# Performance work log

Hardware: AMD Instinct MI355X
Metric: run time of the kernel (lower is better)

## Reference

```python
import jax, jax.numpy as jnp
import numpy as np

N_NODES = 100000
N_EDGES = 1600000
IN_DIM = 128
HEADS = 8
STATE_DIM = 16   # per-head hidden
OUT_DIM = 8      # per-head output
NEG_SLOPE = 0.2


def _gat_conv(x, src, dst, W, a_src, a_dst, b, num_nodes, heads, d):
    # x: [N, F_in]; W: [F_in, heads*d]; a_src/a_dst: [heads, d]; b: [heads*d]
    h = (x @ W).reshape(num_nodes, heads, d)                # [N,H,D]
    s_src = jnp.einsum('nhd,hd->nh', h, a_src)              # [N,H]
    s_dst = jnp.einsum('nhd,hd->nh', h, a_dst)              # [N,H]
    e = jax.nn.leaky_relu(s_src[src] + s_dst[dst], NEG_SLOPE)   # [E,H]
    # segment softmax over edges sharing the same destination node
    m = jax.ops.segment_max(e, dst, num_segments=num_nodes)     # [N,H]
    m = jnp.where(jnp.isfinite(m), m, jnp.zeros_like(m))
    ex = jnp.exp(e - m[dst])                                    # [E,H]
    denom = jax.ops.segment_sum(ex, dst, num_segments=num_nodes)
    alpha = ex / (denom[dst] + 1e-16)                           # [E,H]
    # weighted scatter-aggregate of source features
    out = jax.ops.segment_sum(h[src] * alpha[:, :, None], dst, num_segments=num_nodes)
    return out.reshape(num_nodes, heads * d) + b


def setup_inputs() -> dict:
    key = jax.random.key(0)
    ks = jax.random.split(key, 12)
    x = jax.random.normal(ks[0], (N_NODES, IN_DIM), dtype=jnp.float32)
    edge_index = jax.random.randint(ks[1], (2, N_EDGES), 0, N_NODES, dtype=jnp.int64)
    s1 = 1.0 / np.sqrt(IN_DIM)
    s2 = 1.0 / np.sqrt(HEADS * STATE_DIM)
    W1 = jax.random.normal(ks[2], (IN_DIM, HEADS * STATE_DIM), dtype=jnp.float32) * s1
    a1_src = jax.random.normal(ks[3], (HEADS, STATE_DIM), dtype=jnp.float32) * s2
    a1_dst = jax.random.normal(ks[4], (HEADS, STATE_DIM), dtype=jnp.float32) * s2
    b1 = jnp.zeros((HEADS * STATE_DIM,), dtype=jnp.float32)
    W2 = jax.random.normal(ks[5], (HEADS * STATE_DIM, HEADS * OUT_DIM), dtype=jnp.float32) * s2
    a2_src = jax.random.normal(ks[6], (HEADS, OUT_DIM), dtype=jnp.float32) * s2
    a2_dst = jax.random.normal(ks[7], (HEADS, OUT_DIM), dtype=jnp.float32) * s2
    b2 = jnp.zeros((HEADS * OUT_DIM,), dtype=jnp.float32)
    return {"x": x, "edge_index": edge_index, "W1": W1, "a1_src": a1_src,
            "a1_dst": a1_dst, "b1": b1, "W2": W2, "a2_src": a2_src,
            "a2_dst": a2_dst, "b2": b2}


def reference(x, edge_index, W1, a1_src, a1_dst, b1, W2, a2_src, a2_dst, b2):
    # PyG GATConv adds self-loops by default
    loops = jnp.arange(N_NODES, dtype=edge_index.dtype)
    src = jnp.concatenate([edge_index[0], loops])
    dst = jnp.concatenate([edge_index[1], loops])
    h = _gat_conv(x, src, dst, W1, a1_src, a1_dst, b1, N_NODES, HEADS, STATE_DIM)
    h = jax.nn.relu(h)  # dropout is identity at eval
    out = _gat_conv(h, src, dst, W2, a2_src, a2_dst, b2, N_NODES, HEADS, OUT_DIM)
    return out  # [N, HEADS*OUT_DIM]
```

## Files before the change

kernel.cpp:

```cpp
#include <hip/hip_runtime.h>
#include <hip/hip_fp16.h>
#include <math.h>

#define N_NODES 100000
#define N_EDGES 1600000
#define IN_DIM 128
#define HEADS 8
#define D1 16
#define D2 8
#define NEG_SLOPE 0.2f

#define NBKT ((N_NODES + 255) / 256)
#define PART_CHUNK 4096
#define BCAP 6144
#define BCSTRIDE 32
#define GEMM1_BLOCKS ((N_NODES + 63) / 64)

typedef _Float16 f16x8 __attribute__((ext_vector_type(8)));
typedef float    f32x4 __attribute__((ext_vector_type(4)));

struct __align__(16) half8 { __half2 a, b, c, d; };

__device__ __forceinline__ f16x8 load_cvt8(const float* p) {
    float4 v0 = *(const float4*)p, v1 = *(const float4*)(p + 4);
    f16x8 r;
    r[0] = (_Float16)v0.x; r[1] = (_Float16)v0.y;
    r[2] = (_Float16)v0.z; r[3] = (_Float16)v0.w;
    r[4] = (_Float16)v1.x; r[5] = (_Float16)v1.y;
    r[6] = (_Float16)v1.z; r[7] = (_Float16)v1.w;
    return r;
}

template<int CTRL>
__device__ __forceinline__ float dpp_add(float x) {
    int y = __builtin_amdgcn_update_dpp(0, __builtin_bit_cast(int, x),
                                        CTRL, 0xF, 0xF, true);
    return x + __builtin_bit_cast(float, y);
}

template<int OUTC, int D, bool XF32>
__device__ __forceinline__ void gemm_body(int gb, const void* __restrict__ Ain,
                                          const __half* __restrict__ Bt,
                                          __half* __restrict__ C,
                                          const float* __restrict__ a_s,
                                          const float* __restrict__ a_d,
                                          float* __restrict__ s_src,
                                          float* __restrict__ s_dst,
                                          int n_rows) {
    constexpr int K = 128;
    constexpr int NT = OUTC / 16;
    int wid  = threadIdx.x >> 6;
    int lane = threadIdx.x & 63;
    int row0 = gb * 64 + wid * 16;
    int lr   = lane & 15;
    int ks   = (lane >> 4) * 8;

    int arow = row0 + lr;
    arow = arow < n_rows ? arow : n_rows - 1;

    f16x8 a0, a1, a2, a3;
    if constexpr (XF32) {
        const float* ap = (const float*)Ain + (long)arow * K + ks;
        a0 = load_cvt8(ap);
        a1 = load_cvt8(ap + 32);
        a2 = load_cvt8(ap + 64);
        a3 = load_cvt8(ap + 96);
    } else {
        const __half* ap = (const __half*)Ain + (long)arow * K + ks;
        a0 = *(const f16x8*)(ap);
        a1 = *(const f16x8*)(ap + 32);
        a2 = *(const f16x8*)(ap + 64);
        a3 = *(const f16x8*)(ap + 96);
    }

    f32x4 acc[NT];
#pragma unroll
    for (int j = 0; j < NT; ++j) acc[j] = (f32x4)(0.f);

#pragma unroll
    for (int j = 0; j < NT; ++j) {
        const __half* bp = Bt + (long)(j * 16 + lr) * K + ks;
        f16x8 b0 = *(const f16x8*)(bp);
        f16x8 b1 = *(const f16x8*)(bp + 32);
        f16x8 b2 = *(const f16x8*)(bp + 64);
        f16x8 b3 = *(const f16x8*)(bp + 96);
        acc[j] = __builtin_amdgcn_mfma_f32_16x16x32_f16(a0, b0, acc[j], 0, 0, 0);
        acc[j] = __builtin_amdgcn_mfma_f32_16x16x32_f16(a1, b1, acc[j], 0, 0, 0);
        acc[j] = __builtin_amdgcn_mfma_f32_16x16x32_f16(a2, b2, acc[j], 0, 0, 0);
        acc[j] = __builtin_amdgcn_mfma_f32_16x16x32_f16(a3, b3, acc[j], 0, 0, 0);
    }

    float asv[NT], adv[NT];
#pragma unroll
    for (int j = 0; j < NT; ++j) {
        asv[j] = a_s[j * 16 + lr];
        adv[j] = a_d[j * 16 + lr];
    }

    __shared__ __half stg[4][16 * OUTC];
    __half* sp_ = stg[wid];

    int rbase4 = (lane >> 4) * 4;
#pragma unroll
    for (int r = 0; r < 4; ++r) {
        int lrow = rbase4 + r;

#pragma unroll
        for (int j = 0; j < NT; ++j)
            sp_[lrow * OUTC + j * 16 + lr] = __float2half(acc[j][r]);

        int rr = row0 + lrow;
        bool valid = rr < n_rows;

        float ps[NT], pd[NT];
#pragma unroll
        for (int j = 0; j < NT; ++j) {
            ps[j] = acc[j][r] * asv[j];
            pd[j] = acc[j][r] * adv[j];
        }
        if constexpr (D == 16) {
#pragma unroll
            for (int j = 0; j < NT; ++j) {
                ps[j] = dpp_add<0x118>(ps[j]); ps[j] = dpp_add<0x114>(ps[j]);
                ps[j] = dpp_add<0x112>(ps[j]); ps[j] = dpp_add<0x111>(ps[j]);
                pd[j] = dpp_add<0x118>(pd[j]); pd[j] = dpp_add<0x114>(pd[j]);
                pd[j] = dpp_add<0x112>(pd[j]); pd[j] = dpp_add<0x111>(pd[j]);
            }
            if (valid && lr == 15) {
                float* sp = s_src + rr * 8;
                float* dp = s_dst + rr * 8;
                *(float4*)(sp)     = make_float4(ps[0], ps[1], ps[2], ps[3]);
                *(float4*)(sp + 4) = make_float4(ps[4], ps[5], ps[6], ps[7]);
                *(float4*)(dp)     = make_float4(pd[0], pd[1], pd[2], pd[3]);
                *(float4*)(dp + 4) = make_float4(pd[4], pd[5], pd[6], pd[7]);
            }
        } else {
#pragma unroll
            for (int j = 0; j < NT; ++j) {
                ps[j] = dpp_add<0x114>(ps[j]); ps[j] = dpp_add<0x112>(ps[j]);
                ps[j] = dpp_add<0x111>(ps[j]);
                pd[j] = dpp_add<0x114>(pd[j]); pd[j] = dpp_add<0x112>(pd[j]);
                pd[j] = dpp_add<0x111>(pd[j]);
            }
            if (valid && lr == 7) {
#pragma unroll
                for (int j = 0; j < NT; ++j) {
                    s_src[rr * 8 + 2 * j] = ps[j];
                    s_dst[rr * 8 + 2 * j] = pd[j];
                }
            }
            if (valid && lr == 15) {
#pragma unroll
                for (int j = 0; j < NT; ++j) {
                    s_src[rr * 8 + 2 * j + 1] = ps[j];
                    s_dst[rr * 8 + 2 * j + 1] = pd[j];
                }
            }
        }
    }

    constexpr int CPR = OUTC / 8;
    constexpr int CPL = 2 * OUTC / 64;
#pragma unroll
    for (int t = 0; t < CPL; ++t) {
        int c = t * 64 + lane;
        int row = c / CPR;
        if (row0 + row < n_rows) {
            half8 v = *(half8*)(sp_ + c * 8);
            *(half8*)(C + (long)row0 * OUTC + c * 8) = v;
        }
    }
}

__global__ __launch_bounds__(256)
void convert_w_kernel(const float* __restrict__ W1, const float* __restrict__ W2,
                      __half* __restrict__ Wt1, __half* __restrict__ Wt2,
                      int* __restrict__ bcursor) {
    int idx = blockIdx.x * 256 + threadIdx.x;
    if (idx < NBKT * BCSTRIDE) bcursor[idx] = 0;
    if (idx < 128 * 128) {
        int k = idx / 128, j = idx % 128;
        Wt1[(long)j * 128 + k] = __float2half(W1[idx]);
    } else {
        int i = idx - 128 * 128;
        if (i < 128 * 64) {
            int k = i / 64, j = i % 64;
            Wt2[(long)j * 128 + k] = __float2half(W2[i]);
        }
    }
}

__global__ __launch_bounds__(256)
void partition_kernel(const int* __restrict__ src, const int* __restrict__ dst,
                      int* __restrict__ bcursor, int2* __restrict__ bpairs) {
    constexpr int EPT = PART_CHUNK / 256;
    __shared__ int hist[NBKT];
    for (int i = threadIdx.x; i < NBKT; i += 256) hist[i] = 0;
    __syncthreads();
    int e0 = blockIdx.x * PART_CHUNK;
    int sv[EPT], dv[EPT];
#pragma unroll
    for (int j = 0; j < EPT; ++j) {
        int e = e0 + j * 256 + threadIdx.x;
        bool ok = e < N_EDGES;
        dv[j] = ok ? dst[e] : -1;
        sv[j] = ok ? src[e] : 0;
    }
#pragma unroll
    for (int j = 0; j < EPT; ++j)
        if (dv[j] >= 0) atomicAdd(&hist[dv[j] >> 8], 1);
    __syncthreads();
    for (int i = threadIdx.x; i < NBKT; i += 256) {
        int c = hist[i];
        if (c) {
            int r = atomicAdd(&bcursor[i * BCSTRIDE], c);
            hist[i] = i * BCAP + (r < BCAP ? r : BCAP);
        }
    }
    __syncthreads();
#pragma unroll
    for (int j = 0; j < EPT; ++j) {
        if (dv[j] >= 0) {
            int bkt = dv[j] >> 8;
            int pos = atomicAdd(&hist[bkt], 1);
            if (pos < (bkt + 1) * BCAP)
                bpairs[pos] = make_int2(sv[j], dv[j]);
        }
    }
}

__global__ __launch_bounds__(256)
void localcsr_gemm1_kernel(const int* __restrict__ bcursor,
                           const int2* __restrict__ bpairs,
                           int* __restrict__ row_start, int* __restrict__ row_end,
                           int* __restrict__ eidx,
                           const float* __restrict__ x, const __half* __restrict__ Wt1,
                           __half* __restrict__ C,
                           const float* __restrict__ a_s, const float* __restrict__ a_d,
                           float* __restrict__ s_src, float* __restrict__ s_dst) {
    if (blockIdx.x >= NBKT) {
        gemm_body<128, D1, true>(blockIdx.x - NBKT, x, Wt1, C,
                                 a_s, a_d, s_src, s_dst, N_NODES);
        return;
    }
    __shared__ int cnt[256];
    __shared__ int sh[256];
    __shared__ int cur[256];
    int b = blockIdx.x;
    int tid = threadIdx.x;
    int n0 = b << 8;
    int m0 = b * BCAP;
    int count = bcursor[b * BCSTRIDE];
    int m1 = m0 + (count < BCAP ? count : BCAP);
    cnt[tid] = 0;
    __syncthreads();
    for (int k = m0 + tid; k < m1; k += 256)
        atomicAdd(&cnt[bpairs[k].y & 255], 1);
    __syncthreads();
    int c = cnt[tid];
    sh[tid] = c;
    __syncthreads();
    int run = c;
    for (int off = 1; off < 256; off <<= 1) {
        int add = (tid >= off) ? sh[tid - off] : 0;
        __syncthreads();
        run += add;
        sh[tid] = run;
        __syncthreads();
    }
    int excl = run - c;
    cur[tid] = m0 + excl;
    if (n0 + tid < N_NODES) {
        row_start[n0 + tid] = m0 + excl;
        row_end[n0 + tid]   = m0 + excl + c;
    }
    __syncthreads();
    for (int k = m0 + tid; k < m1; k += 256) {
        int2 p = bpairs[k];
        int pos = atomicAdd(&cur[p.y & 255], 1);
        eidx[pos] = p.x;
    }
}

__global__ __launch_bounds__(256)
void gemm2_kernel(const __half* __restrict__ A, const __half* __restrict__ Bt,
                  __half* __restrict__ C,
                  const float* __restrict__ a_s, const float* __restrict__ a_d,
                  float* __restrict__ s_src, float* __restrict__ s_dst) {
    gemm_body<64, D2, false>(blockIdx.x, A, Bt, C, a_s, a_d, s_src, s_dst, N_NODES);
}

template<int D, bool RELU, typename OT>
__global__ __launch_bounds__(256)
void aggregate_wave_kernel(const int* __restrict__ rs, const int* __restrict__ re,
                           const int* __restrict__ eidx,
                           const __half* __restrict__ h,
                           const float* __restrict__ ssrc, const float* __restrict__ sdst,
                           const float* __restrict__ bias, OT* __restrict__ out) {
    constexpr int F = HEADS * D;
    constexpr int EPL = F / 64;
    int lane = threadIdx.x & 63;
    int node = blockIdx.x * (256 / 64) + (threadIdx.x >> 6);
    node = __builtin_amdgcn_readfirstlane(node);
    if (node >= N_NODES) return;
    int hd = lane >> 3;
    int esl = lane & 7;

    float sdv = sdst[node * HEADS + hd];
    float sc0 = ssrc[node * HEADS + hd] + sdv;
    float w0 = __expf(sc0 > 0.f ? sc0 : NEG_SLOPE * sc0);
    float wsum = w0;

    float accx, accy = 0.f;
    if constexpr (EPL == 2) {
        float2 v = __half22float2(*(const __half2*)(h + (long)node * F + lane * 2));
        accx = w0 * v.x; accy = w0 * v.y;
    } else {
        accx = w0 * __half2float(h[(long)node * F + lane]);
    }

    int e0 = rs[node], e1 = re[node];
    int e1m1 = e1 - 1;

    for (int e = e0; e < e1; e += 8) {
        int idx = e + esl;
        int ci = idx < e1m1 ? idx : e1m1;
        int s_mine = eidx[ci];
        float sc = ssrc[s_mine * HEADS + hd] + sdv;
        float w_mine = __expf(sc > 0.f ? sc : NEG_SLOPE * sc);
        w_mine = (idx < e1) ? w_mine : 0.f;

        int grp = lane & 56;
#pragma unroll
        for (int i = 0; i < 8; ++i) {
            int si = (int)__builtin_amdgcn_readlane((unsigned)s_mine, i);
            float wi = __shfl(w_mine, grp + i, 64);
            wsum += wi;
            if constexpr (EPL == 2) {
                const __half2* hp = (const __half2*)(h + (long)si * F) + lane;
                float2 v = __half22float2(*hp);
                accx = fmaf(wi, v.x, accx);
                accy = fmaf(wi, v.y, accy);
            } else {
                accx = fmaf(wi, __half2float(h[(long)si * F + lane]), accx);
            }
        }
    }

    float inv = 1.f / (wsum + 1e-16f);
    if constexpr (EPL == 2) {
        float2 b = *(const float2*)(bias + lane * 2);
        float ox = accx * inv + b.x;
        float oy = accy * inv + b.y;
        if (RELU) { ox = fmaxf(ox, 0.f); oy = fmaxf(oy, 0.f); }
        if constexpr (sizeof(OT) == 2) {
            *(__half2*)((__half*)out + (long)node * F + lane * 2) = __floats2half2_rn(ox, oy);
        } else {
            *(float2*)((float*)out + (long)node * F + lane * 2) = make_float2(ox, oy);
        }
    } else {
        float o = accx * inv + bias[lane];
        if (RELU) o = fmaxf(o, 0.f);
        if constexpr (sizeof(OT) == 2) {
            ((__half*)out)[(long)node * F + lane] = __float2half(o);
        } else {
            ((float*)out)[(long)node * F + lane] = o;
        }
    }
}

extern "C" void kernel_launch(void* const* d_in, const int* in_sizes, int n_in,
                              void* d_out, int out_size, void* d_ws, size_t ws_size,
                              hipStream_t stream) {
    const float* x   = (const float*)d_in[0];
    const int*   ei  = (const int*)d_in[1];
    const float* W1  = (const float*)d_in[2];
    const float* a1s = (const float*)d_in[3];
    const float* a1d = (const float*)d_in[4];
    const float* b1  = (const float*)d_in[5];
    const float* W2  = (const float*)d_in[6];
    const float* a2s = (const float*)d_in[7];
    const float* a2d = (const float*)d_in[8];
    const float* b2  = (const float*)d_in[9];
    float* out = (float*)d_out;

    const int* src = ei;
    const int* dst = ei + N_EDGES;

    float* ws = (float*)d_ws;
    float* bufA = ws;
    float* bufB = bufA + (size_t)N_NODES * 128;
    float* ssrc = bufB + (size_t)N_NODES * 128;
    float* sdst = ssrc + (size_t)N_NODES * HEADS;
    int* counts    = (int*)(sdst + (size_t)N_NODES * HEADS);
    int* row_start = counts + N_NODES;
    int* row_end   = row_start + N_NODES + 1;

    int* bcursor = counts + 1024;
    __half* Wt1  = (__half*)(counts + 1024 + NBKT * BCSTRIDE);
    __half* Wt2  = (__half*)(counts + 1024 + NBKT * BCSTRIDE + 8192);
    int2* bpairs  = (int2*)bufB;
    __half* h1out = (__half*)bufB;
    int* eidx = (int*)((char*)bufA + (size_t)32 * 1024 * 1024);

    __half* hbuf = (__half*)bufA;

    convert_w_kernel<<<(128 * 128 + 128 * 64 + 255) / 256, 256, 0, stream>>>(
        W1, W2, Wt1, Wt2, bcursor);
    partition_kernel<<<(N_EDGES + PART_CHUNK - 1) / PART_CHUNK, 256, 0, stream>>>(
        src, dst, bcursor, bpairs);
    localcsr_gemm1_kernel<<<NBKT + GEMM1_BLOCKS, 256, 0, stream>>>(
        bcursor, bpairs, row_start, row_end, eidx,
        x, Wt1, hbuf, a1s, a1d, ssrc, sdst);
    aggregate_wave_kernel<D1, true, __half><<<(N_NODES + 3) / 4, 256, 0, stream>>>(
        row_start, row_end, eidx, hbuf, ssrc, sdst, b1, h1out);
    gemm2_kernel<<<GEMM1_BLOCKS, 256, 0, stream>>>(
        h1out, Wt2, hbuf, a2s, a2d, ssrc, sdst);
    aggregate_wave_kernel<D2, false, float><<<(N_NODES + 3) / 4, 256, 0, stream>>>(
        row_start, row_end, eidx, hbuf, ssrc, sdst, b2, out);
}
```

Baseline: 324.2 us.

## Split wave across edges with 16-byte feature loads and cross-lane reduction in aggregation

The aggregation kernel previously had all 64 lanes of a wave read one neighbour row at a time, each lane loading 2 or 1 halves. Now each lane loads 8 halves (16 bytes), so one wave covers several neighbour rows in parallel. Each lane keeps 8 partial accumulators, and these are combined across lane groups with xor-shuffle reductions at the end. The intent is fewer, wider gather loads and fewer serial iterations per edge group, paid for with extra shuffles, more registers and only the first lanes doing the output store.

```diff
diff --git a/kernel.cpp b/kernel.cpp
--- a/kernel.cpp
+++ b/kernel.cpp
@@ -298,26 +298,29 @@
                            const float* __restrict__ ssrc, const float* __restrict__ sdst,
                            const float* __restrict__ bias, OT* __restrict__ out) {
     constexpr int F = HEADS * D;
-    constexpr int EPL = F / 64;
+    constexpr int LPE = F / 8;
+    constexpr int EPI = 64 / LPE;
+    constexpr int GPI = 8 / EPI;
     int lane = threadIdx.x & 63;
-    int node = blockIdx.x * (256 / 64) + (threadIdx.x >> 6);
+    int node = blockIdx.x * 4 + (threadIdx.x >> 6);
     node = __builtin_amdgcn_readfirstlane(node);
     if (node >= N_NODES) return;
-    int hd = lane >> 3;
+
+    int hd  = lane >> 3;
     int esl = lane & 7;
+    int lq  = lane / LPE;
+    int lf  = lane % LPE;
+    int fidx = lf * 8;
+    int hd_f = fidx / D;
 
     float sdv = sdst[node * HEADS + hd];
     float sc0 = ssrc[node * HEADS + hd] + sdv;
-    float w0 = __expf(sc0 > 0.f ? sc0 : NEG_SLOPE * sc0);
-    float wsum = w0;
-
-    float accx, accy = 0.f;
-    if constexpr (EPL == 2) {
-        float2 v = __half22float2(*(const __half2*)(h + (long)node * F + lane * 2));
-        accx = w0 * v.x; accy = w0 * v.y;
-    } else {
-        accx = w0 * __half2float(h[(long)node * F + lane]);
-    }
+    float w0s = __expf(sc0 > 0.f ? sc0 : NEG_SLOPE * sc0);
+    float wsum_s = w0s;
+
+    float acc[8];
+#pragma unroll
+    for (int k = 0; k < 8; ++k) acc[k] = 0.f;
 
     int e0 = rs[node], e1 = re[node];
     int e1m1 = e1 - 1;
@@ -330,41 +333,69 @@
         float w_mine = __expf(sc > 0.f ? sc : NEG_SLOPE * sc);
         w_mine = (idx < e1) ? w_mine : 0.f;
 
-        int grp = lane & 56;
-#pragma unroll
-        for (int i = 0; i < 8; ++i) {
-            int si = (int)__builtin_amdgcn_readlane((unsigned)s_mine, i);
-            float wi = __shfl(w_mine, grp + i, 64);
-            wsum += wi;
-            if constexpr (EPL == 2) {
-                const __half2* hp = (const __half2*)(h + (long)si * F) + lane;
-                float2 v = __half22float2(*hp);
-                accx = fmaf(wi, v.x, accx);
-                accy = fmaf(wi, v.y, accy);
-            } else {
-                accx = fmaf(wi, __half2float(h[(long)si * F + lane]), accx);
-            }
-        }
-    }
-
+        float gw = w_mine;
+        gw += __shfl_xor(gw, 1, 64);
+        gw += __shfl_xor(gw, 2, 64);
+        gw += __shfl_xor(gw, 4, 64);
+        wsum_s += gw;
+
+#pragma unroll
+        for (int t = 0; t < GPI; ++t) {
+            int i = t * EPI + lq;
+            int si = __shfl(s_mine, i, 64);
+            float wi = __shfl(w_mine, hd_f * 8 + i, 64);
+            half8 v = *(const half8*)(h + (long)si * F + fidx);
+            float2 f0 = __half22float2(v.a), f1 = __half22float2(v.b);
+            float2 f2 = __half22float2(v.c), f3 = __half22float2(v.d);
+            acc[0] = fmaf(wi, f0.x, acc[0]); acc[1] = fmaf(wi, f0.y, acc[1]);
+            acc[2] = fmaf(wi, f1.x, acc[2]); acc[3] = fmaf(wi, f1.y, acc[3]);
+            acc[4] = fmaf(wi, f2.x, acc[4]); acc[5] = fmaf(wi, f2.y, acc[5]);
+            acc[6] = fmaf(wi, f3.x, acc[6]); acc[7] = fmaf(wi, f3.y, acc[7]);
+        }
+    }
+
+#pragma unroll
+    for (int s = LPE; s < 64; s <<= 1) {
+#pragma unroll
+        for (int k = 0; k < 8; ++k)
+            acc[k] += __shfl_xor(acc[k], s, 64);
+    }
+
+    float w0 = __shfl(w0s, hd_f * 8, 64);
+    {
+        half8 v = *(const half8*)(h + (long)node * F + fidx);
+        float2 f0 = __half22float2(v.a), f1 = __half22float2(v.b);
+        float2 f2 = __half22float2(v.c), f3 = __half22float2(v.d);
+        acc[0] = fmaf(w0, f0.x, acc[0]); acc[1] = fmaf(w0, f0.y, acc[1]);
+        acc[2] = fmaf(w0, f1.x, acc[2]); acc[3] = fmaf(w0, f1.y, acc[3]);
+        acc[4] = fmaf(w0, f2.x, acc[4]); acc[5] = fmaf(w0, f2.y, acc[5]);
+        acc[6] = fmaf(w0, f3.x, acc[6]); acc[7] = fmaf(w0, f3.y, acc[7]);
+    }
+
+    float wsum = __shfl(wsum_s, hd_f * 8, 64);
     float inv = 1.f / (wsum + 1e-16f);
-    if constexpr (EPL == 2) {
-        float2 b = *(const float2*)(bias + lane * 2);
-        float ox = accx * inv + b.x;
-        float oy = accy * inv + b.y;
-        if (RELU) { ox = fmaxf(ox, 0.f); oy = fmaxf(oy, 0.f); }
+
+    if (lane < LPE) {
+        float b[8];
+        *(float4*)(b)     = *(const float4*)(bias + fidx);
+        *(float4*)(b + 4) = *(const float4*)(bias + fidx + 4);
+        float o[8];
+#pragma unroll
+        for (int k = 0; k < 8; ++k) {
+            o[k] = acc[k] * inv + b[k];
+            if (RELU) o[k] = fmaxf(o[k], 0.f);
+        }
         if constexpr (sizeof(OT) == 2) {
-            *(__half2*)((__half*)out + (long)node * F + lane * 2) = __floats2half2_rn(ox, oy);
+            half8 hv;
+            hv.a = __floats2half2_rn(o[0], o[1]);
+            hv.b = __floats2half2_rn(o[2], o[3]);
+            hv.c = __floats2half2_rn(o[4], o[5]);
+            hv.d = __floats2half2_rn(o[6], o[7]);
+            *(half8*)((__half*)out + (long)node * F + fidx) = hv;
         } else {
-            *(float2*)((float*)out + (long)node * F + lane * 2) = make_float2(ox, oy);
-        }
-    } else {
-        float o = accx * inv + bias[lane];
-        if (RELU) o = fmaxf(o, 0.f);
-        if constexpr (sizeof(OT) == 2) {
-            ((__half*)out)[(long)node * F + lane] = __float2half(o);
-        } else {
-            ((float*)out)[(long)node * F + lane] = o;
+            float* op = (float*)out + (long)node * F + fidx;
+            *(float4*)(op)     = make_float4(o[0], o[1], o[2], o[3]);
+            *(float4*)(op + 4) = make_float4(o[4], o[5], o[6], o[7]);
         }
     }
 }
```

New measurement: 330.8 us. 2.0% more time.
